# Performance work log

Hardware: AMD Instinct MI355X
Metric: run time of the kernel (lower is better)

The kernel has to match this reference:

```python
import jax, jax.numpy as jnp
import numpy as np


def setup_inputs() -> dict:
    key = jax.random.key(0)
    ks = jax.random.split(key, 7)
    B, T, I, H, O = 256, 512, 64, 512, 24
    s_ih = 1.0 / np.sqrt(H)
    return {
        "x":    jax.random.normal(ks[0], (B, T, I), dtype=jnp.float32),
        "W_ih": jax.random.normal(ks[1], (H, I), dtype=jnp.float32) * s_ih,
        "W_hh": jax.random.normal(ks[2], (H, H), dtype=jnp.float32) * s_ih,
        "b_ih": jax.random.normal(ks[3], (H,), dtype=jnp.float32) * s_ih,
        "b_hh": jax.random.normal(ks[4], (H,), dtype=jnp.float32) * s_ih,
        "fc_w": jax.random.normal(ks[5], (O, H), dtype=jnp.float32) * s_ih,
        "fc_b": jax.random.normal(ks[6], (O,), dtype=jnp.float32) * s_ih,
    }


def reference(x, W_ih, W_hh, b_ih, b_hh, fc_w, fc_b):
    # PyTorch nn.RNN(nonlinearity='relu', batch_first=True):
    #   h_t = relu(x_t @ W_ih^T + b_ih + h_{t-1} @ W_hh^T + b_hh), h_0 = 0
    B, T, I = x.shape
    H = W_hh.shape[0]
    # Precompute input projections for all timesteps in one GEMM: [B, T, H]
    xw = jnp.einsum('bti,hi->bth', x, W_ih) + (b_ih + b_hh)

    def step(h, xw_t):
        h = jax.nn.relu(xw_t + h @ W_hh.T)  # [B, H]
        return h, None

    h0 = jnp.zeros((B, H), dtype=x.dtype)
    h_last, _ = jax.lax.scan(step, h0, jnp.swapaxes(xw, 0, 1))  # scan over T
    # Final linear on last timestep's hidden state: [B, O]
    return h_last @ fc_w.T + fc_b
```

## Files before the change

kernel.cpp:

```cpp
#include <hip/hip_runtime.h>


#define T_STEPS 512
#define NG      16
#define NM      8
#define SLAB    32768
#define FLAGS_OFF (2 * NG * SLAB)
#define POLL_CAP 100000
#define TAG_CAP  20000

#define LA_STRIDE 1040
#define LA_PLANE  16640
#define LA_PAR    33280
#define LX_OFF    66560
#define LX_STRIDE 144
#define LX_PLANE  2304

typedef short          short8  __attribute__((ext_vector_type(8)));
typedef unsigned short bfx4    __attribute__((ext_vector_type(4)));
typedef unsigned       uintx4  __attribute__((ext_vector_type(4)));
typedef float          floatx4 __attribute__((ext_vector_type(4)));
typedef unsigned long long ull;

__device__ __forceinline__ unsigned short f2bf(float x) {
    unsigned u = __float_as_uint(x);
    u = (u + 0x7fffu + ((u >> 16) & 1u)) >> 16;
    return (unsigned short)u;
}
__device__ __forceinline__ float bf2f(unsigned short h) {
    return __uint_as_float(((unsigned)h) << 16);
}
__device__ __forceinline__ unsigned cvtpk(float a, float b) {
    unsigned r;
    asm("v_cvt_pk_bf16_f32 %0, %1, %2" : "=v"(r) : "v"(a), "v"(b));
    return r;
}
__device__ __forceinline__ void pack_hilo(float f0, float f1, float f2, float f3,
                                          ull& hi, ull& lo) {
    const unsigned h01 = cvtpk(f0, f1), h23 = cvtpk(f2, f3);
    const float l0 = f0 - __uint_as_float(h01 << 16);
    const float l1 = f1 - __uint_as_float(h01 & 0xffff0000u);
    const float l2 = f2 - __uint_as_float(h23 << 16);
    const float l3 = f3 - __uint_as_float(h23 & 0xffff0000u);
    const unsigned q01 = cvtpk(l0, l1), q23 = cvtpk(l2, l3);
    hi = (ull)h01 | ((ull)h23 << 32);
    lo = (ull)q01 | ((ull)q23 << 32);
}
__device__ __forceinline__ void st_ag_u32(void* p, unsigned v) {
    __hip_atomic_store((unsigned*)p, v, __ATOMIC_RELAXED, __HIP_MEMORY_SCOPE_AGENT);
}
__device__ __forceinline__ unsigned ld_ag_u32(const void* p) {
    return __hip_atomic_load((const unsigned*)p, __ATOMIC_RELAXED, __HIP_MEMORY_SCOPE_AGENT);
}
__device__ __forceinline__ uintx4 ld_ag_b128_async(const void* p) {
    uintx4 v;
    asm volatile("global_load_dwordx4 %0, %1, off sc1"
                 : "=v"(v) : "v"(p) : "memory");
    return v;
}
__device__ __forceinline__ void st_ag_b32(void* p, unsigned v) {
    asm volatile("global_store_dword %0, %1, off sc1"
                 :: "v"(p), "v"(v) : "memory");
}
__device__ __forceinline__ void st_ag_b128(void* p, uintx4 v) {
    asm volatile("global_store_dwordx4 %0, %1, off sc1"
                 :: "v"(p), "v"(v) : "memory");
}
__device__ __forceinline__ void wait_vm0() {
    asm volatile("s_waitcnt vmcnt(0)" ::: "memory");
}
__device__ __forceinline__ void poll_flag(const unsigned* p, unsigned want) {
    int it = 0;
    for (;;) {
        unsigned f = ld_ag_u32(p);
        if (f == want || f == want + 1u) return;
        if (++it >= POLL_CAP) return;
    }
}

__global__ __launch_bounds__(256, 1) void rnn_persistent(
    const float* __restrict__ x,     const float* __restrict__ W_ih,
    const float* __restrict__ W_hh,  const float* __restrict__ b_ih,
    const float* __restrict__ b_hh,  const float* __restrict__ fc_w,
    const float* __restrict__ fc_b,  float* __restrict__ out,
    unsigned char* __restrict__ ws)
{
    const int tid  = threadIdx.x;
    const int lane = tid & 63;
    const int w    = tid >> 6;
    const int n    = lane & 15;
    const int quad = lane >> 4;

    const int bid = blockIdx.x;
    const int g = bid >> 3;
    const int m = bid & 7;

    unsigned char* ex = (unsigned char*)ws;
    unsigned* flagbase = (unsigned*)(ex + FLAGS_OFF + g * 64);
    __shared__ __align__(16) unsigned char smem[LX_OFF + 2 * LX_PLANE];

    const int wrow = m * 64 + w * 16 + n;
    short8 Whi[18], Wlo[18];
    #pragma unroll
    for (int kt = 0; kt < 18; ++kt) {
        const float* p = (kt < 16) ? (W_hh + wrow * 512 + kt * 32 + quad * 8)
                                   : (W_ih + wrow * 64 + (kt - 16) * 32 + quad * 8);
        #pragma unroll
        for (int jj = 0; jj < 8; ++jj) {
            float f = p[jj];
            unsigned short h = f2bf(f);
            Whi[kt][jj] = (short)h;
            Wlo[kt][jj] = (short)f2bf(f - bf2f(h));
        }
    }
    const float bias_i = b_ih[wrow] + b_hh[wrow];

    const int prow = tid >> 4, pc4 = tid & 15;
    int poff[7];
    #pragma unroll
    for (int r = 0; r < 7; ++r) {
        const int pm = r + (r >= m ? 1 : 0);
        poff[r] = prow * 2048 + pm * 256 + pc4 * 16;
    }

    {
        uintx4 z = {0u, 0u, 0u, 0u};
        st_ag_b128(ex + g * SLAB + prow * 2048 + m * 256 + pc4 * 16, z);
        #pragma unroll
        for (int r = 0; r < 4; ++r) {
            const int row = quad * 4 + r;
            *(unsigned short*)(smem + 0 * LA_PLANE + row * LA_STRIDE + wrow * 2) = 0;
            *(unsigned short*)(smem + LA_PLANE + row * LA_STRIDE + wrow * 2) = 0;
        }
    }
    wait_vm0();
    __syncthreads();
    if (tid == 0) st_ag_u32(flagbase + m, 1u);

    const int xrow = tid >> 4, xi4 = tid & 15;
    const float* xbase = x + (size_t)(g * 16 + xrow) * T_STEPS * 64 + xi4 * 4;
    float4 xv_cur = *(const float4*)(xbase + 0 * 64);
    for (int t = 0; t < T_STEPS; ++t) {
        const unsigned texp = (((unsigned)t >> 1) & 1u) << 31;
        const unsigned char* slab_r = ex + ((t & 1) * NG + g) * SLAB;

        uintx4 P[7];
        #pragma unroll
        for (int r = 0; r < 7; ++r) P[r] = ld_ag_b128_async(slab_r + poff[r]);

        if (tid < 7) {
            const int pm = tid + (tid >= m ? 1 : 0);
            poll_flag(flagbase + pm, (unsigned)t + 1u);
        }
        wait_vm0();
        __syncthreads();

        {
            int it = 0;
            for (;;) {
                unsigned bad = 0;
                #pragma unroll
                for (int r = 0; r < 7; ++r)
                    bad |= (P[r].x ^ texp) | (P[r].y ^ texp)
                         | (P[r].z ^ texp) | (P[r].w ^ texp);
                if (!(bad & 0x80000000u) || ++it >= TAG_CAP) break;
                #pragma unroll
                for (int r = 0; r < 7; ++r) P[r] = ld_ag_b128_async(slab_r + poff[r]);
                wait_vm0();
            }
        }

        const int tn = (t + 1 < T_STEPS) ? (t + 1) : (T_STEPS - 1);
        const float4 xv_nxt = *(const float4*)(xbase + (size_t)tn * 64);

        unsigned char* abase = smem + (t & 1) * LA_PAR;
        #pragma unroll
        for (int r = 0; r < 7; ++r) {
            const int pm = r + (r >= m ? 1 : 0);
            ull hi, lo;
            pack_hilo(__uint_as_float(P[r].x & 0x7fffffffu),
                      __uint_as_float(P[r].y & 0x7fffffffu),
                      __uint_as_float(P[r].z & 0x7fffffffu),
                      __uint_as_float(P[r].w & 0x7fffffffu), hi, lo);
            const int base = prow * LA_STRIDE + pm * 128 + pc4 * 8;
            *(ull*)(abase + base)            = hi;
            *(ull*)(abase + LA_PLANE + base) = lo;
        }
        {
            ull hi, lo;
            pack_hilo(xv_cur.x, xv_cur.y, xv_cur.z, xv_cur.w, hi, lo);
            *(ull*)(smem + LX_OFF + xrow * LX_STRIDE + xi4 * 8)            = hi;
            *(ull*)(smem + LX_OFF + LX_PLANE + xrow * LX_STRIDE + xi4 * 8) = lo;
        }
        __syncthreads();

        floatx4 c0 = {0.f,0.f,0.f,0.f}, c1 = {0.f,0.f,0.f,0.f}, c2 = {0.f,0.f,0.f,0.f};
        #pragma unroll
        for (int kt = 0; kt < 16; ++kt) {
            const unsigned char* ba = abase + n * LA_STRIDE + kt * 64 + quad * 16;
            short8 ah = *(const short8*)(ba);
            short8 al = *(const short8*)(ba + LA_PLANE);
            c0 = __builtin_amdgcn_mfma_f32_16x16x32_bf16(ah, Whi[kt], c0, 0, 0, 0);
            c1 = __builtin_amdgcn_mfma_f32_16x16x32_bf16(al, Whi[kt], c1, 0, 0, 0);
            c2 = __builtin_amdgcn_mfma_f32_16x16x32_bf16(ah, Wlo[kt], c2, 0, 0, 0);
        }
        #pragma unroll
        for (int kt = 16; kt < 18; ++kt) {
            const unsigned char* ba = smem + LX_OFF + n * LX_STRIDE + (kt - 16) * 64 + quad * 16;
            short8 ah = *(const short8*)(ba);
            short8 al = *(const short8*)(ba + LX_PLANE);
            c0 = __builtin_amdgcn_mfma_f32_16x16x32_bf16(ah, Whi[kt], c0, 0, 0, 0);
            c1 = __builtin_amdgcn_mfma_f32_16x16x32_bf16(al, Whi[kt], c1, 0, 0, 0);
            c2 = __builtin_amdgcn_mfma_f32_16x16x32_bf16(ah, Wlo[kt], c2, 0, 0, 0);
        }

        const unsigned otag = ((((unsigned)t + 1u) >> 1) & 1u) << 31;
        unsigned char* slab_w = ex + (((t + 1) & 1) * NG + g) * SLAB;
        unsigned char* obase  = smem + ((t + 1) & 1) * LA_PAR;
        const floatx4 cs = c0 + c1 + c2;
        const int r0 = quad * 4;
        {
            const float v0 = fmaxf(cs[0] + bias_i, 0.f);
            const float v1 = fmaxf(cs[1] + bias_i, 0.f);
            const float v2 = fmaxf(cs[2] + bias_i, 0.f);
            const float v3 = fmaxf(cs[3] + bias_i, 0.f);
            st_ag_b32(slab_w + (r0+0) * 2048 + wrow * 4, __float_as_uint(v0) | otag);
            st_ag_b32(slab_w + (r0+1) * 2048 + wrow * 4, __float_as_uint(v1) | otag);
            st_ag_b32(slab_w + (r0+2) * 2048 + wrow * 4, __float_as_uint(v2) | otag);
            st_ag_b32(slab_w + (r0+3) * 2048 + wrow * 4, __float_as_uint(v3) | otag);
            const unsigned h01 = cvtpk(v0, v1), h23 = cvtpk(v2, v3);
            const float l0 = v0 - __uint_as_float(h01 << 16);
            const float l1 = v1 - __uint_as_float(h01 & 0xffff0000u);
            const float l2 = v2 - __uint_as_float(h23 << 16);
            const float l3 = v3 - __uint_as_float(h23 & 0xffff0000u);
            const unsigned q01 = cvtpk(l0, l1), q23 = cvtpk(l2, l3);
            *(unsigned short*)(obase + (r0+0) * LA_STRIDE + wrow * 2) = (unsigned short)(h01 & 0xffffu);
            *(unsigned short*)(obase + (r0+1) * LA_STRIDE + wrow * 2) = (unsigned short)(h01 >> 16);
            *(unsigned short*)(obase + (r0+2) * LA_STRIDE + wrow * 2) = (unsigned short)(h23 & 0xffffu);
            *(unsigned short*)(obase + (r0+3) * LA_STRIDE + wrow * 2) = (unsigned short)(h23 >> 16);
            *(unsigned short*)(obase + LA_PLANE + (r0+0) * LA_STRIDE + wrow * 2) = (unsigned short)(q01 & 0xffffu);
            *(unsigned short*)(obase + LA_PLANE + (r0+1) * LA_STRIDE + wrow * 2) = (unsigned short)(q01 >> 16);
            *(unsigned short*)(obase + LA_PLANE + (r0+2) * LA_STRIDE + wrow * 2) = (unsigned short)(q23 & 0xffffu);
            *(unsigned short*)(obase + LA_PLANE + (r0+3) * LA_STRIDE + wrow * 2) = (unsigned short)(q23 >> 16);
        }
        if (tid == 0) st_ag_u32(flagbase + m, (unsigned)t + 2u);
        xv_cur = xv_nxt;
    }

    if (m != 0) return;
    {
        const unsigned texp = 0;
        const unsigned char* slab_r = ex + (0 * NG + g) * SLAB;
        uintx4 P[7];
        #pragma unroll
        for (int r = 0; r < 7; ++r) P[r] = ld_ag_b128_async(slab_r + poff[r]);
        if (tid < 7) poll_flag(flagbase + (tid + 1), (unsigned)T_STEPS + 1u);
        wait_vm0();
        __syncthreads();
        int it = 0;
        for (;;) {
            unsigned bad = 0;
            #pragma unroll
            for (int r = 0; r < 7; ++r)
                bad |= (P[r].x ^ texp) | (P[r].y ^ texp)
                     | (P[r].z ^ texp) | (P[r].w ^ texp);
            if (!(bad & 0x80000000u) || ++it >= TAG_CAP) break;
            #pragma unroll
            for (int r = 0; r < 7; ++r) P[r] = ld_ag_b128_async(slab_r + poff[r]);
            wait_vm0();
        }
        unsigned char* abase = smem;
        #pragma unroll
        for (int r = 0; r < 7; ++r) {
            const int pm = r + 1;
            ull hi, lo;
            pack_hilo(__uint_as_float(P[r].x & 0x7fffffffu),
                      __uint_as_float(P[r].y & 0x7fffffffu),
                      __uint_as_float(P[r].z & 0x7fffffffu),
                      __uint_as_float(P[r].w & 0x7fffffffu), hi, lo);
            const int base = prow * LA_STRIDE + pm * 128 + pc4 * 8;
            *(ull*)(abase + base)            = hi;
            *(ull*)(abase + LA_PLANE + base) = lo;
        }
    }
    __syncthreads();
    for (int idx = tid; idx < 384; idx += 256) {
        const int row = idx / 24, o = idx % 24;
        const float* wp = fc_w + o * 512;
        float s = 0.f;
        for (int k = 0; k < 512; k += 4) {
            bfx4 hv = *(const bfx4*)(smem + row * LA_STRIDE + k * 2);
            bfx4 lv = *(const bfx4*)(smem + LA_PLANE + row * LA_STRIDE + k * 2);
            const float4 wv = *(const float4*)(wp + k);
            s += (bf2f(hv[0]) + bf2f(lv[0])) * wv.x;
            s += (bf2f(hv[1]) + bf2f(lv[1])) * wv.y;
            s += (bf2f(hv[2]) + bf2f(lv[2])) * wv.z;
            s += (bf2f(hv[3]) + bf2f(lv[3])) * wv.w;
        }
        out[(g * 16 + row) * 24 + o] = s + fc_b[o];
    }
}

extern "C" void kernel_launch(void* const* d_in, const int* in_sizes, int n_in,
                              void* d_out, int out_size, void* d_ws, size_t ws_size,
                              hipStream_t stream) {
    (void)in_sizes; (void)n_in; (void)out_size; (void)ws_size;
    const float* x    = (const float*)d_in[0];
    const float* W_ih = (const float*)d_in[1];
    const float* W_hh = (const float*)d_in[2];
    const float* b_ih = (const float*)d_in[3];
    const float* b_hh = (const float*)d_in[4];
    const float* fc_w = (const float*)d_in[5];
    const float* fc_b = (const float*)d_in[6];
    rnn_persistent<<<NG * NM, 256, 0, stream>>>(x, W_ih, W_hh, b_ih, b_hh,
                                                fc_w, fc_b, (float*)d_out,
                                                (unsigned char*)d_ws);
}
```

Before: 1.463 ms.

## Prefetch next-step peer slab and flags before storing; split MFMA accumulators

The loads of the next timestep's peer hidden-state slab and the peer flags are now issued speculatively right after the activations are computed, before this block's own stores. If the prefetched flag already shows readiness, the following iteration skips polling. The flag store is moved earlier, and the K loop now feeds two independent accumulator sets to shorten the MFMA dependency chain. The data prefetched early may be stale, which leans on the existing tag-bit retry loop and adds extra global traffic.

Measured after the change: 1.938 ms. +32.5%, slower.

```diff
diff --git a/kernel.cpp b/kernel.cpp
--- a/kernel.cpp
+++ b/kernel.cpp
@@ -58,6 +58,12 @@
                  : "=v"(v) : "v"(p) : "memory");
     return v;
 }
+__device__ __forceinline__ unsigned ld_flag_async(const unsigned* p) {
+    unsigned v;
+    asm volatile("global_load_dword %0, %1, off sc1"
+                 : "=v"(v) : "v"(p) : "memory");
+    return v;
+}
 __device__ __forceinline__ void st_ag_b32(void* p, unsigned v) {
     asm volatile("global_store_dword %0, %1, off sc1"
                  :: "v"(p), "v"(v) : "memory");
@@ -77,6 +83,8 @@
         if (++it >= POLL_CAP) return;
     }
 }
+
+#define MFMA_BF16 __builtin_amdgcn_mfma_f32_16x16x32_bf16
 
 __global__ __launch_bounds__(256, 1) void rnn_persistent(
     const float* __restrict__ x,     const float* __restrict__ W_ih,
@@ -140,20 +148,32 @@
     const int xrow = tid >> 4, xi4 = tid & 15;
     const float* xbase = x + (size_t)(g * 16 + xrow) * T_STEPS * 64 + xi4 * 4;
     float4 xv_cur = *(const float4*)(xbase + 0 * 64);
+
+    uintx4 P[7];
+    unsigned Fpre = 0u;
+
     for (int t = 0; t < T_STEPS; ++t) {
         const unsigned texp = (((unsigned)t >> 1) & 1u) << 31;
         const unsigned char* slab_r = ex + ((t & 1) * NG + g) * SLAB;
-
-        uintx4 P[7];
-        #pragma unroll
-        for (int r = 0; r < 7; ++r) P[r] = ld_ag_b128_async(slab_r + poff[r]);
-
+        const unsigned want = (unsigned)t + 1u;
+
+        wait_vm0();
+        __builtin_amdgcn_sched_barrier(0);
         if (tid < 7) {
-            const int pm = tid + (tid >= m ? 1 : 0);
-            poll_flag(flagbase + pm, (unsigned)t + 1u);
-        }
-        wait_vm0();
+            const bool ok = (t > 0) && (Fpre == want || Fpre == want + 1u);
+            if (!ok) {
+                const int pm = tid + (tid >= m ? 1 : 0);
+                poll_flag(flagbase + pm, want);
+            }
+        }
         __syncthreads();
+
+        if (t == 0) {
+            #pragma unroll
+            for (int r = 0; r < 7; ++r) P[r] = ld_ag_b128_async(slab_r + poff[r]);
+            wait_vm0();
+            __builtin_amdgcn_sched_barrier(0);
+        }
 
         {
             int it = 0;
@@ -194,40 +214,63 @@
         }
         __syncthreads();
 
-        floatx4 c0 = {0.f,0.f,0.f,0.f}, c1 = {0.f,0.f,0.f,0.f}, c2 = {0.f,0.f,0.f,0.f};
-        #pragma unroll
-        for (int kt = 0; kt < 16; ++kt) {
+        floatx4 c0a = {0.f,0.f,0.f,0.f}, c1a = {0.f,0.f,0.f,0.f}, c2a = {0.f,0.f,0.f,0.f};
+        floatx4 c0b = {0.f,0.f,0.f,0.f}, c1b = {0.f,0.f,0.f,0.f}, c2b = {0.f,0.f,0.f,0.f};
+        #pragma unroll
+        for (int kt = 0; kt < 8; ++kt) {
             const unsigned char* ba = abase + n * LA_STRIDE + kt * 64 + quad * 16;
             short8 ah = *(const short8*)(ba);
             short8 al = *(const short8*)(ba + LA_PLANE);
-            c0 = __builtin_amdgcn_mfma_f32_16x16x32_bf16(ah, Whi[kt], c0, 0, 0, 0);
-            c1 = __builtin_amdgcn_mfma_f32_16x16x32_bf16(al, Whi[kt], c1, 0, 0, 0);
-            c2 = __builtin_amdgcn_mfma_f32_16x16x32_bf16(ah, Wlo[kt], c2, 0, 0, 0);
+            c0a = MFMA_BF16(ah, Whi[kt], c0a, 0, 0, 0);
+            c1a = MFMA_BF16(al, Whi[kt], c1a, 0, 0, 0);
+            c2a = MFMA_BF16(ah, Wlo[kt], c2a, 0, 0, 0);
+        }
+        #pragma unroll
+        for (int kt = 8; kt < 16; ++kt) {
+            const unsigned char* ba = abase + n * LA_STRIDE + kt * 64 + quad * 16;
+            short8 ah = *(const short8*)(ba);
+            short8 al = *(const short8*)(ba + LA_PLANE);
+            c0b = MFMA_BF16(ah, Whi[kt], c0b, 0, 0, 0);
+            c1b = MFMA_BF16(al, Whi[kt], c1b, 0, 0, 0);
+            c2b = MFMA_BF16(ah, Wlo[kt], c2b, 0, 0, 0);
         }
         #pragma unroll
         for (int kt = 16; kt < 18; ++kt) {
             const unsigned char* ba = smem + LX_OFF + n * LX_STRIDE + (kt - 16) * 64 + quad * 16;
             short8 ah = *(const short8*)(ba);
             short8 al = *(const short8*)(ba + LX_PLANE);
-            c0 = __builtin_amdgcn_mfma_f32_16x16x32_bf16(ah, Whi[kt], c0, 0, 0, 0);
-            c1 = __builtin_amdgcn_mfma_f32_16x16x32_bf16(al, Whi[kt], c1, 0, 0, 0);
-            c2 = __builtin_amdgcn_mfma_f32_16x16x32_bf16(ah, Wlo[kt], c2, 0, 0, 0);
-        }
+            c0a = MFMA_BF16(ah, Whi[kt], c0a, 0, 0, 0);
+            c1a = MFMA_BF16(al, Whi[kt], c1a, 0, 0, 0);
+            c2a = MFMA_BF16(ah, Wlo[kt], c2a, 0, 0, 0);
+        }
+        const floatx4 cs = (c0a + c0b) + ((c1a + c1b) + (c2a + c2b));
 
         const unsigned otag = ((((unsigned)t + 1u) >> 1) & 1u) << 31;
         unsigned char* slab_w = ex + (((t + 1) & 1) * NG + g) * SLAB;
         unsigned char* obase  = smem + ((t + 1) & 1) * LA_PAR;
-        const floatx4 cs = c0 + c1 + c2;
         const int r0 = quad * 4;
         {
             const float v0 = fmaxf(cs[0] + bias_i, 0.f);
             const float v1 = fmaxf(cs[1] + bias_i, 0.f);
             const float v2 = fmaxf(cs[2] + bias_i, 0.f);
             const float v3 = fmaxf(cs[3] + bias_i, 0.f);
+
+            if (t + 1 < T_STEPS) {
+                #pragma unroll
+                for (int r = 0; r < 7; ++r)
+                    P[r] = ld_ag_b128_async(slab_w + poff[r]);
+                if (tid < 7) {
+                    const int pm7 = tid + (tid >= m ? 1 : 0);
+                    Fpre = ld_flag_async(flagbase + pm7);
+                }
+            }
+
             st_ag_b32(slab_w + (r0+0) * 2048 + wrow * 4, __float_as_uint(v0) | otag);
             st_ag_b32(slab_w + (r0+1) * 2048 + wrow * 4, __float_as_uint(v1) | otag);
             st_ag_b32(slab_w + (r0+2) * 2048 + wrow * 4, __float_as_uint(v2) | otag);
             st_ag_b32(slab_w + (r0+3) * 2048 + wrow * 4, __float_as_uint(v3) | otag);
+            if (tid == 0) st_ag_u32(flagbase + m, (unsigned)t + 2u);
+
             const unsigned h01 = cvtpk(v0, v1), h23 = cvtpk(v2, v3);
             const float l0 = v0 - __uint_as_float(h01 << 16);
             const float l1 = v1 - __uint_as_float(h01 & 0xffff0000u);
@@ -243,7 +286,6 @@
             *(unsigned short*)(obase + LA_PLANE + (r0+2) * LA_STRIDE + wrow * 2) = (unsigned short)(q23 & 0xffffu);
             *(unsigned short*)(obase + LA_PLANE + (r0+3) * LA_STRIDE + wrow * 2) = (unsigned short)(q23 >> 16);
         }
-        if (tid == 0) st_ag_u32(flagbase + m, (unsigned)t + 2u);
         xv_cur = xv_nxt;
     }
 
@@ -251,9 +293,9 @@
     {
         const unsigned texp = 0;
         const unsigned char* slab_r = ex + (0 * NG + g) * SLAB;
-        uintx4 P[7];
-        #pragma unroll
-        for (int r = 0; r < 7; ++r) P[r] = ld_ag_b128_async(slab_r + poff[r]);
+        uintx4 Pf[7];
+        #pragma unroll
+        for (int r = 0; r < 7; ++r) Pf[r] = ld_ag_b128_async(slab_r + poff[r]);
         if (tid < 7) poll_flag(flagbase + (tid + 1), (unsigned)T_STEPS + 1u);
         wait_vm0();
         __syncthreads();
@@ -262,11 +304,11 @@
             unsigned bad = 0;
             #pragma unroll
             for (int r = 0; r < 7; ++r)
-                bad |= (P[r].x ^ texp) | (P[r].y ^ texp)
-                     | (P[r].z ^ texp) | (P[r].w ^ texp);
+                bad |= (Pf[r].x ^ texp) | (Pf[r].y ^ texp)
+                     | (Pf[r].z ^ texp) | (Pf[r].w ^ texp);
             if (!(bad & 0x80000000u) || ++it >= TAG_CAP) break;
             #pragma unroll
-            for (int r = 0; r < 7; ++r) P[r] = ld_ag_b128_async(slab_r + poff[r]);
+            for (int r = 0; r < 7; ++r) Pf[r] = ld_ag_b128_async(slab_r + poff[r]);
             wait_vm0();
         }
         unsigned char* abase = smem;
@@ -274,10 +316,10 @@
         for (int r = 0; r < 7; ++r) {
             const int pm = r + 1;
             ull hi, lo;
-            pack_hilo(__uint_as_float(P[r].x & 0x7fffffffu),
-                      __uint_as_float(P[r].y & 0x7fffffffu),
-                      __uint_as_float(P[r].z & 0x7fffffffu),
-                      __uint_as_float(P[r].w & 0x7fffffffu), hi, lo);
+            pack_hilo(__uint_as_float(Pf[r].x & 0x7fffffffu),
+                      __uint_as_float(Pf[r].y & 0x7fffffffu),
+                      __uint_as_float(Pf[r].z & 0x7fffffffu),
+                      __uint_as_float(Pf[r].w & 0x7fffffffu), hi, lo);
             const int base = prow * LA_STRIDE + pm * 128 + pc4 * 8;
             *(ull*)(abase + base)            = hi;
             *(ull*)(abase + LA_PLANE + base) = lo;
```
